# Optimization experiments

Measured on AMD Instinct MI355X. Metric: run time of the kernel, lower is better.

## Reference

```python
import jax, jax.numpy as jnp
import numpy as np

D_MODEL, D_STATE, EXPAND = 256, 16, 2
D_INNER = EXPAND * D_MODEL
DT_RANK = (D_MODEL + 15) // 16
BATCH, SEQLEN = 4, 4096


def silu(x):
    return x * jax.nn.sigmoid(x)


def setup_inputs() -> dict:
    key = jax.random.key(0)
    ks = jax.random.split(key, 10)
    h = jax.random.normal(ks[0], (BATCH, SEQLEN, D_MODEL), dtype=jnp.float32)
    Wi_f = jax.random.normal(ks[1], (2 * D_INNER, D_MODEL), dtype=jnp.float32) / np.sqrt(D_MODEL)
    Wi_b = jax.random.normal(ks[2], (2 * D_INNER, D_MODEL), dtype=jnp.float32) / np.sqrt(D_MODEL)
    Wx_f = jax.random.normal(ks[3], (DT_RANK + 2 * D_STATE, D_INNER), dtype=jnp.float32) / np.sqrt(D_INNER)
    Wx_b = jax.random.normal(ks[4], (DT_RANK + 2 * D_STATE, D_INNER), dtype=jnp.float32) / np.sqrt(D_INNER)
    dt_std = DT_RANK ** -0.5
    Wdt_f = jax.random.uniform(ks[5], (D_INNER, DT_RANK), dtype=jnp.float32, minval=-dt_std, maxval=dt_std)
    Wdt_b = jax.random.uniform(ks[6], (D_INNER, DT_RANK), dtype=jnp.float32, minval=-dt_std, maxval=dt_std)
    # dt bias = inverse-softplus of dt sampled log-uniform in [1e-3, 1e-1]
    dt = jnp.exp(jax.random.uniform(ks[7], (D_INNER,), dtype=jnp.float32) * (np.log(0.1) - np.log(0.001)) + np.log(0.001))
    dt = jnp.clip(dt, 1e-4, None)
    inv_dt = dt + jnp.log(-jnp.expm1(-dt))
    bdt_f = inv_dt
    bdt_b = inv_dt
    A_log = jnp.log(jnp.broadcast_to(jnp.arange(1, D_STATE + 1, dtype=jnp.float32), (D_INNER, D_STATE)))
    A_log_f = A_log
    A_log_b = A_log
    D_f = jnp.ones((D_INNER,), dtype=jnp.float32)
    D_b = jnp.ones((D_INNER,), dtype=jnp.float32)
    Wo = jax.random.normal(ks[8], (D_MODEL, 2 * D_INNER), dtype=jnp.float32) / np.sqrt(2 * D_INNER)
    return {"hidden_states": h, "Wi_f": Wi_f, "Wi_b": Wi_b, "Wx_f": Wx_f, "Wx_b": Wx_b,
            "Wdt_f": Wdt_f, "Wdt_b": Wdt_b, "bdt_f": bdt_f, "bdt_b": bdt_b,
            "A_log_f": A_log_f, "A_log_b": A_log_b, "D_f": D_f, "D_b": D_b, "Wo": Wo}


def mamba_dir(h, Wi, Wx, Wdt, bdt, A_log, Dp, reverse):
    b, l, _ = h.shape
    di, r = Wdt.shape
    n = A_log.shape[1]
    xz = h @ Wi.T                      # [b,l,2*di]
    if reverse:
        xz = xz[:, ::-1]
    x, z = xz[..., :di], xz[..., di:]
    u = silu(x)                        # selective_scan input u
    x_dbl = u @ Wx.T                   # [b,l,r+2n]
    delta = jax.nn.softplus(x_dbl[..., :r] @ Wdt.T + bdt)   # [b,l,di]
    Bm = x_dbl[..., r:r + n]           # [b,l,n]
    Cm = x_dbl[..., r + n:r + 2 * n]   # [b,l,n]
    A = -jnp.exp(A_log)                # [di,n]

    def step(s, inp):
        u_t, d_t, B_t, C_t = inp       # [b,di],[b,di],[b,n],[b,n]
        dA = jnp.exp(d_t[..., None] * A)                         # [b,di,n]
        s = dA * s + (d_t * u_t)[..., None] * B_t[:, None, :]    # [b,di,n]
        y_t = jnp.einsum('bdn,bn->bd', s, C_t)
        return s, y_t

    s0 = jnp.zeros((b, di, n), dtype=u.dtype)
    xs = (jnp.swapaxes(u, 0, 1), jnp.swapaxes(delta, 0, 1),
          jnp.swapaxes(Bm, 0, 1), jnp.swapaxes(Cm, 0, 1))
    _, ys = jax.lax.scan(step, s0, xs)
    y = jnp.swapaxes(ys, 0, 1) + u * Dp          # skip term D*u
    y = y * silu(z)                              # gated output
    if reverse:
        y = y[:, ::-1]
    return y


def reference(hidden_states, Wi_f, Wi_b, Wx_f, Wx_b, Wdt_f, Wdt_b, bdt_f, bdt_b, A_log_f, A_log_b, D_f, D_b, Wo):
    y_f = mamba_dir(hidden_states, Wi_f, Wx_f, Wdt_f, bdt_f, A_log_f, D_f, False)
    y_b = mamba_dir(hidden_states, Wi_b, Wx_b, Wdt_b, bdt_b, A_log_b, D_b, True)
    y = jnp.concatenate([y_f, y_b], axis=-1)     # [b,l,2*di]
    return y @ Wo.T                              # [b,l,d_model]
```

## Files before the change

kernel.cpp:

```cpp
#include <hip/hip_runtime.h>
#include <hip/hip_bf16.h>
#include <cstddef>
#include <cstdint>

#define D_MODELc 256
#define D_STATEc 16
#define D_INNERc 512
#define DT_RANKc 16
#define BATCHc   4
#define SEQLENc  4096
#define NCHUNK   128
#define CHUNK    32

typedef unsigned short u16;
typedef __attribute__((ext_vector_type(8))) short bf16x8;
typedef __attribute__((ext_vector_type(4))) float f32x4;
typedef float __attribute__((ext_vector_type(4))) f4v;

__device__ __forceinline__ float siluf(float v) { return v / (1.f + __expf(-v)); }

__device__ __forceinline__ u16 bf16_rne(float f) {
    uint32_t u = __float_as_uint(f);
    u += 0x7fffu + ((u >> 16) & 1u);
    return (u16)(u >> 16);
}
__device__ __forceinline__ float bf16_to_f(u16 h) {
    return __uint_as_float(((uint32_t)h) << 16);
}
__device__ __forceinline__ uint32_t pack_hl(float f) {
    u16 hh = bf16_rne(f);
    u16 ll = bf16_rne(f - bf16_to_f(hh));
    return ((uint32_t)hh << 16) | ll;
}
__device__ __forceinline__ float unpack_add(uint32_t v) {
    return __uint_as_float(v & 0xFFFF0000u) + __uint_as_float(v << 16);
}
__device__ __forceinline__ void unpack_frag(const uint32_t* q, bf16x8& fh, bf16x8& fl) {
    union { bf16x8 v; uint32_t w[4]; } H, L;
    #pragma unroll
    for (int i = 0; i < 4; i++) {
        uint32_t a = q[2 * i], b = q[2 * i + 1];
        H.w[i] = (a >> 16) | (b & 0xFFFF0000u);
        L.w[i] = (a & 0xFFFFu) | (b << 16);
    }
    fh = H.v; fl = L.v;
}
__device__ __forceinline__ float softplusf(float x) {
    return fmaxf(x, 0.f) + __logf(1.f + __expf(-fabsf(x)));
}
__device__ __forceinline__ float dot16_tree(const f4v x[4], const float* w, float bias) {
    float t0 = fmaf(x[0][1], w[1],  x[0][0] * w[0]);
    float t1 = fmaf(x[0][3], w[3],  x[0][2] * w[2]);
    float t2 = fmaf(x[1][1], w[5],  x[1][0] * w[4]);
    float t3 = fmaf(x[1][3], w[7],  x[1][2] * w[6]);
    float t4 = fmaf(x[2][1], w[9],  x[2][0] * w[8]);
    float t5 = fmaf(x[2][3], w[11], x[2][2] * w[10]);
    float t6 = fmaf(x[3][1], w[13], x[3][2] * 0.f + x[3][0] * w[12]);
    float t7 = fmaf(x[3][3], w[15], x[3][2] * w[14]);
    return bias + (((t0 + t1) + (t2 + t3)) + ((t4 + t5) + (t6 + t7)));
}
__device__ __forceinline__ void qladder(float q, float* qd) {
    float q2 = q * q;
    float q4 = q2 * q2;
    float q8 = q4 * q4;
    qd[0] = q;        qd[1] = q2;       qd[2] = q2 * q;   qd[3] = q4;
    qd[4] = q4 * q;   qd[5] = q4 * q2;  qd[6] = q4 * qd[2]; qd[7] = q8;
    qd[8] = q8 * q;   qd[9] = q8 * q2;  qd[10] = q8 * qd[2]; qd[11] = q8 * q4;
    qd[12] = q8 * qd[4]; qd[13] = q8 * qd[5]; qd[14] = q8 * qd[6]; qd[15] = q8 * q8;
}

#define GLL16(g, l) __builtin_amdgcn_global_load_lds( \
    (const __attribute__((address_space(1))) uint32_t*)(g), \
    (__attribute__((address_space(3))) uint32_t*)(l), 16, 0, 0)

__global__ __launch_bounds__(256) void split_kernel(const float* __restrict__ in,
                                                    u16* __restrict__ hi,
                                                    u16* __restrict__ lo, int n4) {
    int i = blockIdx.x * 256 + threadIdx.x;
    const int stride = gridDim.x * 256;
    for (; i < n4; i += stride) {
        float4 v = ((const float4*)in)[i];
        u16 h0 = bf16_rne(v.x), h1 = bf16_rne(v.y), h2 = bf16_rne(v.z), h3 = bf16_rne(v.w);
        ushort4 hv; hv.x = h0; hv.y = h1; hv.z = h2; hv.w = h3;
        ushort4 lv;
        lv.x = bf16_rne(v.x - bf16_to_f(h0));
        lv.y = bf16_rne(v.y - bf16_to_f(h1));
        lv.z = bf16_rne(v.z - bf16_to_f(h2));
        lv.w = bf16_rne(v.w - bf16_to_f(h3));
        ((ushort4*)hi)[i] = hv;
        ((ushort4*)lo)[i] = lv;
    }
}

template<int EPI, int NBL2, int AINT>
__global__ __launch_bounds__(256) void gemm_mfma(
        const u16* __restrict__ Ah, const u16* __restrict__ Al, int lda,
        const u16* __restrict__ Bh, const u16* __restrict__ Bl, int ldb,
        float* __restrict__ out0,
        uint32_t* __restrict__ uhl,
        int M, int N, int K) {
    __shared__ u16 ldsB[2][2][4][128][8];
    const int t    = threadIdx.x;
    const int lane = t & 63;
    const int wid  = t >> 6;
    const int wrow = wid >> 1, wcol = wid & 1;

    const int id  = blockIdx.x;
    const int xcd = id & 7;
    const int j   = id >> 3;
    const int nb  = j & ((1 << NBL2) - 1);
    const int mg  = j >> NBL2;
    const int m0  = (mg * 8 + xcd) * 128;
    const int n0  = nb * 128;

    const int lr  = lane & 15;
    const int kgl = lane >> 4;

    f32x4 acc[4][4] = {};

    auto stageB = [&](int buf, int k0) {
        #pragma unroll
        for (int i = 0; i < 4; i++) {
            int c    = i * 256 + t;
            int tile = c >> 9;
            int kg   = (c >> 7) & 3;
            int row  = c & 127;
            const u16* bsrc = tile ? Bl : Bh;
            const u16* g = bsrc + (size_t)(n0 + row) * ldb + k0 + kg * 8;
            GLL16(g, ((char*)ldsB) + (size_t)buf * 16384 + (size_t)c * 16);
        }
    };

    const int NT = K >> 5;
    stageB(0, 0);
    __syncthreads();

    for (int kt = 0; kt < NT; ++kt) {
        const int buf = kt & 1;
        if (kt + 1 < NT) stageB(buf ^ 1, (kt + 1) * 32);

        bf16x8 afh[4], afl[4];
        const int k0 = kt * 32;
        #pragma unroll
        for (int mi = 0; mi < 4; mi++) {
            int row = m0 + wrow * 64 + mi * 16 + lr;
            if (AINT == 0) {
                afh[mi] = *(const bf16x8*)(Ah + (size_t)row * lda + k0 + kgl * 8);
                afl[mi] = *(const bf16x8*)(Al + (size_t)row * lda + k0 + kgl * 8);
            } else {
                const uint32_t* Aint = (const uint32_t*)Ah;
                unpack_frag(Aint + (size_t)row * lda + k0 + kgl * 8, afh[mi], afl[mi]);
            }
        }

        #pragma unroll
        for (int ni = 0; ni < 4; ni++) {
            int row = wcol * 64 + ni * 16 + lr;
            bf16x8 bfh = *(const bf16x8*)&ldsB[buf][0][kgl][row][0];
            bf16x8 bfl = *(const bf16x8*)&ldsB[buf][1][kgl][row][0];
            #pragma unroll
            for (int mi = 0; mi < 4; mi++) {
                acc[mi][ni] = __builtin_amdgcn_mfma_f32_16x16x32_bf16(afh[mi], bfh, acc[mi][ni], 0, 0, 0);
                acc[mi][ni] = __builtin_amdgcn_mfma_f32_16x16x32_bf16(afh[mi], bfl, acc[mi][ni], 0, 0, 0);
                acc[mi][ni] = __builtin_amdgcn_mfma_f32_16x16x32_bf16(afl[mi], bfh, acc[mi][ni], 0, 0, 0);
            }
        }
        __syncthreads();
    }

    #pragma unroll
    for (int mi = 0; mi < 4; mi++) {
        #pragma unroll
        for (int ni = 0; ni < 4; ni++) {
            #pragma unroll
            for (int r = 0; r < 4; r++) {
                int m = m0 + wrow * 64 + mi * 16 + kgl * 4 + r;
                int n = n0 + wcol * 64 + ni * 16 + lr;
                float v = acc[mi][ni][r];
                if (EPI == 0) {
                    __builtin_nontemporal_store(v, &out0[(size_t)m * N + n]);
                } else {
                    float s = siluf(v);
                    int dirn = n >> 10;
                    int nn   = n & 1023;
                    size_t dof = (size_t)dirn * (size_t)M * 512;
                    if (nn < 512) {
                        uhl[dof + (size_t)m * 512 + nn] = pack_hl(s);
                    } else {
                        out0[dof + (size_t)m * 512 + (nn - 512)] = s;
                    }
                }
            }
        }
    }
}

__global__ __launch_bounds__(256) void xdbl_mfma(
        const uint32_t* __restrict__ Uhl,
        const u16* __restrict__ WxH, const u16* __restrict__ WxL,
        float* __restrict__ out) {
    __shared__ uint32_t lds[4][64][8];
    const int t    = threadIdx.x;
    const int lane = t & 63;
    const int wid  = t >> 6;
    const int m0   = blockIdx.x * 64;
    const int dir  = blockIdx.y;
    const int Mp   = gridDim.x * 64;
    const int lr   = lane & 15;
    const int kgl  = lane >> 4;

    const size_t dofU = (size_t)dir * (size_t)Mp * 512;
    const size_t dofW = (size_t)dir * (size_t)48 * 512;

    f32x4 acc[3] = {};

    for (int k0 = 0; k0 < 512; k0 += 32) {
        #pragma unroll
        for (int i = 0; i < 2; i++) {
            int c    = i * 256 + t;
            int kg   = c >> 7;
            int row  = (c >> 1) & 63;
            int half = c & 1;
            const uint32_t* g = Uhl + dofU + (size_t)(m0 + row) * 512 + k0 + kg * 8 + half * 4;
            GLL16(g, ((char*)lds) + (size_t)c * 16);
        }
        __syncthreads();

        bf16x8 afh, afl;
        unpack_frag(&lds[kgl][wid * 16 + lr][0], afh, afl);
        #pragma unroll
        for (int nf = 0; nf < 3; nf++) {
            const size_t boff = dofW + (size_t)(nf * 16 + lr) * 512 + k0 + kgl * 8;
            bf16x8 bfh = *(const bf16x8*)(WxH + boff);
            bf16x8 bfl = *(const bf16x8*)(WxL + boff);
            acc[nf] = __builtin_amdgcn_mfma_f32_16x16x32_bf16(afh, bfh, acc[nf], 0, 0, 0);
            acc[nf] = __builtin_amdgcn_mfma_f32_16x16x32_bf16(afh, bfl, acc[nf], 0, 0, 0);
            acc[nf] = __builtin_amdgcn_mfma_f32_16x16x32_bf16(afl, bfh, acc[nf], 0, 0, 0);
        }
        __syncthreads();
    }

    float* o = out + (size_t)dir * (size_t)Mp * 48;
    #pragma unroll
    for (int nf = 0; nf < 3; nf++) {
        #pragma unroll
        for (int r = 0; r < 4; r++) {
            int m = m0 + wid * 16 + kgl * 4 + r;
            int n = nf * 16 + lr;
            o[(size_t)m * 48 + n] = acc[nf][r];
        }
    }
}

__global__ __launch_bounds__(256) void scan_phaseA(
        const uint32_t* __restrict__ Uhl,
        const float* __restrict__ XD,
        const float* __restrict__ Wdt_f, const float* __restrict__ Wdt_b,
        const float* __restrict__ bdt_f, const float* __restrict__ bdt_b,
        const float* __restrict__ AL_f, const float* __restrict__ AL_b,
        float* __restrict__ SDL, float* __restrict__ S) {
    const int c   = blockIdx.x;
    const int d   = blockIdx.y * 256 + threadIdx.x;
    const int z   = blockIdx.z;
    const int dir = z & 1;
    const int b   = z >> 1;
    const int PB  = gridDim.z >> 1;
    const int Mp  = PB * SEQLENc;
    const float* Wdt = dir ? Wdt_b : Wdt_f;
    const float* bdt = dir ? bdt_b : bdt_f;
    const float* AL  = dir ? AL_b  : AL_f;
    const uint32_t* UD = Uhl + (size_t)dir * Mp * 512;
    const float* XDD = XD + (size_t)dir * Mp * 48;

    float w[16], a[16], s[16];
    #pragma unroll
    for (int n = 0; n < 16; n++) {
        w[n] = Wdt[d * 16 + n];
        a[n] = -__expf(AL[d * 16 + n]);
        s[n] = 0.f;
    }
    const float a0 = a[0];
    bool pw = (a0 != 0.f);
    #pragma unroll
    for (int n = 1; n < 16; n++)
        pw = pw && (fabsf(a[n] - (float)(n + 1) * a0) <= 3e-6f * fabsf(a[n]));
    const float bb = bdt[d];
    float sdl = 0.f;

    for (int i = 0; i < CHUNK; i++) {
        int tt = c * CHUNK + i;
        int l  = dir ? (SEQLENc - 1 - tt) : tt;
        size_t row = (size_t)b * SEQLENc + l;
        float uu = unpack_add(UD[row * 512 + d]);
        const f4v* xr4 = (const f4v*)&XDD[row * 48];
        f4v xw[4] = {xr4[0], xr4[1], xr4[2], xr4[3]};
        float dl = softplusf(dot16_tree(xw, w, bb));
        sdl += dl;
        float du = dl * uu;
        if (pw) {
            float qd[16];
            qladder(__expf(a0 * dl), qd);
            #pragma unroll
            for (int g = 0; g < 4; g++) {
                f4v B4 = xr4[4 + g];
                #pragma unroll
                for (int jj = 0; jj < 4; jj++) {
                    int n = g * 4 + jj;
                    s[n] = fmaf(qd[n], s[n], du * B4[jj]);
                }
            }
        } else {
            #pragma unroll
            for (int g = 0; g < 4; g++) {
                f4v B4 = xr4[4 + g];
                #pragma unroll
                for (int jj = 0; jj < 4; jj++) {
                    int n = g * 4 + jj;
                    float dA = __expf(dl * a[n]);
                    s[n] = fmaf(dA, s[n], du * B4[jj]);
                }
            }
        }
    }
    SDL[((size_t)z * NCHUNK + c) * 512 + d] = sdl;
    size_t base = (((size_t)z * NCHUNK + c) * 16) * 512 + d;
    #pragma unroll
    for (int n = 0; n < 16; n++)
        S[base + (size_t)n * 512] = s[n];
}

__global__ __launch_bounds__(256) void scan_phaseB(const float* __restrict__ SDL,
                                                   float* __restrict__ S,
                                                   const float* __restrict__ AL_f,
                                                   const float* __restrict__ AL_b) {
    const int g   = blockIdx.x * 256 + threadIdx.x;
    const int d   = g & 511;
    const int n   = (g >> 9) & 15;
    const int z   = g >> 13;
    const int dir = z & 1;
    const float an = -__expf((dir ? AL_b : AL_f)[d * 16 + n]);
    const size_t strideS = (size_t)16 * 512;
    size_t offS = (((size_t)z * NCHUNK) * 16 + n) * 512 + d;
    size_t offD = ((size_t)z * NCHUNK) * 512 + d;
    float carry = 0.f;
    float sdl = SDL[offD], ss = S[offS];
    for (int c = 0; c < NCHUNK; c++) {
        float sdn = 0.f, sn = 0.f;
        if (c + 1 < NCHUNK) { sdn = SDL[offD + 512]; sn = S[offS + strideS]; }
        float pp = __expf(an * sdl);
        S[offS] = carry;
        carry = pp * carry + ss;
        sdl = sdn; ss = sn;
        offS += strideS; offD += 512;
    }
}

__global__ __launch_bounds__(256) void scan_phaseC(
        const uint32_t* __restrict__ Uhl,
        const float* __restrict__ XD,
        const float* __restrict__ Wdt_f, const float* __restrict__ Wdt_b,
        const float* __restrict__ bdt_f, const float* __restrict__ bdt_b,
        const float* __restrict__ AL_f, const float* __restrict__ AL_b,
        const float* __restrict__ E,
        const float* __restrict__ SZ,
        const float* __restrict__ D_f,  const float* __restrict__ D_b,
        uint32_t* __restrict__ Yhl) {
    const int c   = blockIdx.x;
    const int d   = blockIdx.y * 256 + threadIdx.x;
    const int z   = blockIdx.z;
    const int dir = z & 1;
    const int b   = z >> 1;
    const int PB  = gridDim.z >> 1;
    const int Mp  = PB * SEQLENc;
    const float* Wdt = dir ? Wdt_b : Wdt_f;
    const float* bdt = dir ? bdt_b : bdt_f;
    const float* AL  = dir ? AL_b  : AL_f;
    const uint32_t* UD = Uhl + (size_t)dir * Mp * 512;
    const float* XDD = XD + (size_t)dir * Mp * 48;
    const float* SZD = SZ + (size_t)dir * Mp * 512;

    float w[16], a[16], s[16];
    size_t base = (((size_t)z * NCHUNK + c) * 16) * 512 + d;
    #pragma unroll
    for (int n = 0; n < 16; n++) {
        w[n] = Wdt[d * 16 + n];
        a[n] = -__expf(AL[d * 16 + n]);
        s[n] = E[base + (size_t)n * 512];
    }
    const float a0 = a[0];
    bool pw = (a0 != 0.f);
    #pragma unroll
    for (int n = 1; n < 16; n++)
        pw = pw && (fabsf(a[n] - (float)(n + 1) * a0) <= 3e-6f * fabsf(a[n]));
    const float bb = bdt[d];
    const float Dd = (dir ? D_b : D_f)[d];

    for (int i = 0; i < CHUNK; i++) {
        int tt = c * CHUNK + i;
        int l  = dir ? (SEQLENc - 1 - tt) : tt;
        size_t row = (size_t)b * SEQLENc + l;
        float uu = unpack_add(UD[row * 512 + d]);
        const f4v* xr4 = (const f4v*)&XDD[row * 48];
        f4v xw[4] = {xr4[0], xr4[1], xr4[2], xr4[3]};
        float dl = softplusf(dot16_tree(xw, w, bb));
        float du = dl * uu;
        float yp0 = 0.f, yp1 = 0.f, yp2 = 0.f, yp3 = 0.f;
        if (pw) {
            float qd[16];
            qladder(__expf(a0 * dl), qd);
            #pragma unroll
            for (int g = 0; g < 4; g++) {
                f4v B4 = xr4[4 + g];
                f4v C4 = xr4[8 + g];
                float yp = 0.f;
                #pragma unroll
                for (int jj = 0; jj < 4; jj++) {
                    int n = g * 4 + jj;
                    s[n] = fmaf(qd[n], s[n], du * B4[jj]);
                    yp = fmaf(s[n], C4[jj], yp);
                }
                if (g == 0) yp0 = yp; else if (g == 1) yp1 = yp;
                else if (g == 2) yp2 = yp; else yp3 = yp;
            }
        } else {
            #pragma unroll
            for (int g = 0; g < 4; g++) {
                f4v B4 = xr4[4 + g];
                f4v C4 = xr4[8 + g];
                float yp = 0.f;
                #pragma unroll
                for (int jj = 0; jj < 4; jj++) {
                    int n = g * 4 + jj;
                    float dA = __expf(dl * a[n]);
                    s[n] = fmaf(dA, s[n], du * B4[jj]);
                    yp = fmaf(s[n], C4[jj], yp);
                }
                if (g == 0) yp0 = yp; else if (g == 1) yp1 = yp;
                else if (g == 2) yp2 = yp; else yp3 = yp;
            }
        }
        float y = (yp0 + yp1) + (yp2 + yp3);
        float sz = SZD[row * 512 + d];
        float yv = (y + uu * Dd) * sz;
        Yhl[row * 1024 + (size_t)dir * 512 + d] = pack_hl(yv);
    }
}

extern "C" void kernel_launch(void* const* d_in, const int* in_sizes, int n_in,
                              void* d_out, int out_size, void* d_ws, size_t ws_size,
                              hipStream_t stream) {
    const float* h    = (const float*)d_in[0];
    const float* Wi_f = (const float*)d_in[1];
    const float* Wi_b = (const float*)d_in[2];
    const float* Wx_f = (const float*)d_in[3];
    const float* Wx_b = (const float*)d_in[4];
    const float* Wdt_f= (const float*)d_in[5];
    const float* Wdt_b= (const float*)d_in[6];
    const float* bdt_f= (const float*)d_in[7];
    const float* bdt_b= (const float*)d_in[8];
    const float* Al_f = (const float*)d_in[9];
    const float* Al_b = (const float*)d_in[10];
    const float* D_f  = (const float*)d_in[11];
    const float* D_b  = (const float*)d_in[12];
    const float* Wo   = (const float*)d_in[13];
    float* out = (float*)d_out;

    const size_t W_ELE  = 1024 * 256;
    const size_t WX_ELE = 48 * 512;
    const size_t FB   = (size_t)SEQLENc * D_INNERc;
    const size_t FH   = (size_t)SEQLENc * D_MODELc;
    const size_t FX   = (size_t)SEQLENc * 48;
    const size_t FP   = (size_t)NCHUNK * 16 * 512;
    const size_t FD   = (size_t)NCHUNK * 512;
    const size_t FY   = (size_t)SEQLENc * 1024;

    const size_t fixed_bytes = (8 * W_ELE + 4 * WX_ELE) * sizeof(u16);
    const size_t per_b = 2 * FH * sizeof(u16)
                       + 2 * FB * sizeof(float)
                       + 2 * FB * sizeof(uint32_t)
                       + 2 * FX * sizeof(float)
                       + 2 * (FP + FD) * sizeof(float)
                       + FY * sizeof(uint32_t);
    int PB = 4;
    if (fixed_bytes + 4 * per_b + 65536 > ws_size) PB = 2;
    if (fixed_bytes + 2 * per_b + 65536 > ws_size) PB = 1;

    char* cur = (char*)d_ws;
    auto alloc = [&](size_t bytes) -> char* {
        char* p = cur; cur += (bytes + 255) & ~(size_t)255; return p;
    };
    u16* WiH = (u16*)alloc(2 * W_ELE * 2);
    u16* WiL = (u16*)alloc(2 * W_ELE * 2);
    u16* WoH = (u16*)alloc(W_ELE * 2);
    u16* WoL = (u16*)alloc(W_ELE * 2);
    u16* WxH = (u16*)alloc(2 * WX_ELE * 2);
    u16* WxL = (u16*)alloc(2 * WX_ELE * 2);
    u16*      hH  = (u16*)alloc((size_t)PB * FH * 2);
    u16*      hL  = (u16*)alloc((size_t)PB * FH * 2);
    float*    sz  = (float*)alloc((size_t)PB * 2 * FB * 4);
    uint32_t* uhl = (uint32_t*)alloc((size_t)PB * 2 * FB * 4);
    float*    xd  = (float*)alloc((size_t)PB * 2 * FX * 4);
    float*    SDL = (float*)alloc((size_t)PB * 2 * FD * 4);
    float*    S   = (float*)alloc((size_t)PB * 2 * FP * 4);
    uint32_t* yhl = (uint32_t*)alloc((size_t)PB * FY * 4);

    {
        int n4 = (int)(W_ELE / 4);
        int blocks = (n4 + 255) / 256; if (blocks > 1024) blocks = 1024;
        split_kernel<<<blocks, 256, 0, stream>>>(Wi_f, WiH, WiL, n4);
        split_kernel<<<blocks, 256, 0, stream>>>(Wi_b, WiH + W_ELE, WiL + W_ELE, n4);
        split_kernel<<<blocks, 256, 0, stream>>>(Wo,   WoH, WoL, n4);
        int nx4 = (int)(WX_ELE / 4);
        split_kernel<<<(nx4 + 255) / 256, 256, 0, stream>>>(Wx_f, WxH, WxL, nx4);
        split_kernel<<<(nx4 + 255) / 256, 256, 0, stream>>>(Wx_b, WxH + WX_ELE, WxL + WX_ELE, nx4);
    }

    for (int b0 = 0; b0 < BATCHc; b0 += PB) {
        const int Mp = PB * SEQLENc;
        const int MB = Mp / 128;
        const float* hB = h   + (size_t)b0 * FH;
        float*       oB = out + (size_t)b0 * FH;

        {
            int n4 = (int)((size_t)PB * FH / 4);
            int blocks = (n4 + 255) / 256; if (blocks > 2048) blocks = 2048;
            split_kernel<<<blocks, 256, 0, stream>>>(hB, hH, hL, n4);
        }

        gemm_mfma<1, 4, 0><<<16 * MB, 256, 0, stream>>>(
            hH, hL, D_MODELc, WiH, WiL, D_MODELc,
            sz, uhl, Mp, 2048, D_MODELc);

        xdbl_mfma<<<dim3(Mp / 64, 2), 256, 0, stream>>>(uhl, WxH, WxL, xd);

        scan_phaseA<<<dim3(NCHUNK, 2, 2 * PB), 256, 0, stream>>>(
            uhl, xd, Wdt_f, Wdt_b, bdt_f, bdt_b, Al_f, Al_b, SDL, S);
        scan_phaseB<<<PB * 64, 256, 0, stream>>>(SDL, S, Al_f, Al_b);
        scan_phaseC<<<dim3(NCHUNK, 2, 2 * PB), 256, 0, stream>>>(
            uhl, xd, Wdt_f, Wdt_b, bdt_f, bdt_b, Al_f, Al_b,
            S, sz, D_f, D_b, yhl);

        gemm_mfma<0, 1, 1><<<2 * MB, 256, 0, stream>>>(
            (const u16*)yhl, nullptr, 1024, WoH, WoL, 1024,
            oB, nullptr, Mp, D_MODELc, 1024);
    }
}
```

Before: 389.7 us.

## Stage A operand through LDS via async loads and merge weight split launches

```diff
diff --git a/kernel.cpp b/kernel.cpp
--- a/kernel.cpp
+++ b/kernel.cpp
@@ -55,7 +55,7 @@
     float t3 = fmaf(x[1][3], w[7],  x[1][2] * w[6]);
     float t4 = fmaf(x[2][1], w[9],  x[2][0] * w[8]);
     float t5 = fmaf(x[2][3], w[11], x[2][2] * w[10]);
-    float t6 = fmaf(x[3][1], w[13], x[3][2] * 0.f + x[3][0] * w[12]);
+    float t6 = fmaf(x[3][1], w[13], x[3][0] * w[12]);
     float t7 = fmaf(x[3][3], w[15], x[3][2] * w[14]);
     return bias + (((t0 + t1) + (t2 + t3)) + ((t4 + t5) + (t6 + t7)));
 }
@@ -63,7 +63,7 @@
     float q2 = q * q;
     float q4 = q2 * q2;
     float q8 = q4 * q4;
-    qd[0] = q;        qd[1] = q2;       qd[2] = q2 * q;   qd[3] = q4;
+    qd[0] = q;        qd[1] = q2;       qd[2] = q2 * q;     qd[3] = q4;
     qd[4] = q4 * q;   qd[5] = q4 * q2;  qd[6] = q4 * qd[2]; qd[7] = q8;
     qd[8] = q8 * q;   qd[9] = q8 * q2;  qd[10] = q8 * qd[2]; qd[11] = q8 * q4;
     qd[12] = q8 * qd[4]; qd[13] = q8 * qd[5]; qd[14] = q8 * qd[6]; qd[15] = q8 * q8;
@@ -72,6 +72,37 @@
 #define GLL16(g, l) __builtin_amdgcn_global_load_lds( \
     (const __attribute__((address_space(1))) uint32_t*)(g), \
     (__attribute__((address_space(3))) uint32_t*)(l), 16, 0, 0)
+
+__global__ __launch_bounds__(256) void split5_kernel(
+        const float* __restrict__ s0, const float* __restrict__ s1,
+        const float* __restrict__ s2, const float* __restrict__ s3,
+        const float* __restrict__ s4,
+        u16* __restrict__ h0, u16* __restrict__ l0,
+        u16* __restrict__ h1, u16* __restrict__ l1,
+        u16* __restrict__ h2, u16* __restrict__ l2,
+        u16* __restrict__ h3, u16* __restrict__ l3,
+        u16* __restrict__ h4, u16* __restrict__ l4,
+        int n4w, int n4x) {
+    const int which = blockIdx.y;
+    const float* in; u16* hi; u16* lo; int n4;
+    if      (which == 0) { in = s0; hi = h0; lo = l0; n4 = n4w; }
+    else if (which == 1) { in = s1; hi = h1; lo = l1; n4 = n4w; }
+    else if (which == 2) { in = s2; hi = h2; lo = l2; n4 = n4w; }
+    else if (which == 3) { in = s3; hi = h3; lo = l3; n4 = n4x; }
+    else                 { in = s4; hi = h4; lo = l4; n4 = n4x; }
+    for (int i = blockIdx.x * 256 + threadIdx.x; i < n4; i += gridDim.x * 256) {
+        float4 v = ((const float4*)in)[i];
+        u16 a0 = bf16_rne(v.x), a1 = bf16_rne(v.y), a2 = bf16_rne(v.z), a3 = bf16_rne(v.w);
+        ushort4 hv; hv.x = a0; hv.y = a1; hv.z = a2; hv.w = a3;
+        ushort4 lv;
+        lv.x = bf16_rne(v.x - bf16_to_f(a0));
+        lv.y = bf16_rne(v.y - bf16_to_f(a1));
+        lv.z = bf16_rne(v.z - bf16_to_f(a2));
+        lv.w = bf16_rne(v.w - bf16_to_f(a3));
+        ((ushort4*)hi)[i] = hv;
+        ((ushort4*)lo)[i] = lv;
+    }
+}
 
 __global__ __launch_bounds__(256) void split_kernel(const float* __restrict__ in,
                                                     u16* __restrict__ hi,
@@ -80,13 +111,13 @@
     const int stride = gridDim.x * 256;
     for (; i < n4; i += stride) {
         float4 v = ((const float4*)in)[i];
-        u16 h0 = bf16_rne(v.x), h1 = bf16_rne(v.y), h2 = bf16_rne(v.z), h3 = bf16_rne(v.w);
-        ushort4 hv; hv.x = h0; hv.y = h1; hv.z = h2; hv.w = h3;
+        u16 a0 = bf16_rne(v.x), a1 = bf16_rne(v.y), a2 = bf16_rne(v.z), a3 = bf16_rne(v.w);
+        ushort4 hv; hv.x = a0; hv.y = a1; hv.z = a2; hv.w = a3;
         ushort4 lv;
-        lv.x = bf16_rne(v.x - bf16_to_f(h0));
-        lv.y = bf16_rne(v.y - bf16_to_f(h1));
-        lv.z = bf16_rne(v.z - bf16_to_f(h2));
-        lv.w = bf16_rne(v.w - bf16_to_f(h3));
+        lv.x = bf16_rne(v.x - bf16_to_f(a0));
+        lv.y = bf16_rne(v.y - bf16_to_f(a1));
+        lv.z = bf16_rne(v.z - bf16_to_f(a2));
+        lv.w = bf16_rne(v.w - bf16_to_f(a3));
         ((ushort4*)hi)[i] = hv;
         ((ushort4*)lo)[i] = lv;
     }
@@ -99,7 +130,7 @@
         float* __restrict__ out0,
         uint32_t* __restrict__ uhl,
         int M, int N, int K) {
-    __shared__ u16 ldsB[2][2][4][128][8];
+    __shared__ char lds[2][32768];
     const int t    = threadIdx.x;
     const int lane = t & 63;
     const int wid  = t >> 6;
@@ -118,46 +149,75 @@
 
     f32x4 acc[4][4] = {};
 
-    auto stageB = [&](int buf, int k0) {
-        #pragma unroll
-        for (int i = 0; i < 4; i++) {
-            int c    = i * 256 + t;
-            int tile = c >> 9;
-            int kg   = (c >> 7) & 3;
-            int row  = c & 127;
-            const u16* bsrc = tile ? Bl : Bh;
-            const u16* g = bsrc + (size_t)(n0 + row) * ldb + k0 + kg * 8;
-            GLL16(g, ((char*)ldsB) + (size_t)buf * 16384 + (size_t)c * 16);
+    auto stage = [&](int buf, int k0) {
+        if (AINT == 0) {
+            #pragma unroll
+            for (int i = 0; i < 8; i++) {
+                int c    = i * 256 + t;
+                int tile = c >> 9;
+                int kg   = (c >> 7) & 3;
+                int row  = c & 127;
+                const u16* bsrc = (tile == 0) ? Ah : (tile == 1) ? Al : (tile == 2) ? Bh : Bl;
+                int r0 = (tile < 2) ? m0 : n0;
+                int ld = (tile < 2) ? lda : ldb;
+                const u16* g = bsrc + (size_t)(r0 + row) * ld + k0 + kg * 8;
+                GLL16(g, &lds[buf][c * 16]);
+            }
+        } else {
+            const uint32_t* Aint = (const uint32_t*)Ah;
+            #pragma unroll
+            for (int i = 0; i < 8; i++) {
+                int c = i * 256 + t;
+                if (c < 1024) {
+                    int kg   = c >> 8;
+                    int row  = (c >> 1) & 127;
+                    int half = c & 1;
+                    const uint32_t* g = Aint + (size_t)(m0 + row) * lda + k0 + kg * 8 + half * 4;
+                    GLL16(g, &lds[buf][c * 16]);
+                } else {
+                    int cb   = c - 1024;
+                    int tile = cb >> 9;
+                    int kg   = (cb >> 7) & 3;
+                    int row  = cb & 127;
+                    const u16* bsrc = tile ? Bl : Bh;
+                    const u16* g = bsrc + (size_t)(n0 + row) * ldb + k0 + kg * 8;
+                    GLL16(g, &lds[buf][c * 16]);
+                }
+            }
         }
     };
 
     const int NT = K >> 5;
-    stageB(0, 0);
+    stage(0, 0);
     __syncthreads();
 
     for (int kt = 0; kt < NT; ++kt) {
         const int buf = kt & 1;
-        if (kt + 1 < NT) stageB(buf ^ 1, (kt + 1) * 32);
+        if (kt + 1 < NT) stage(buf ^ 1, (kt + 1) * 32);
 
         bf16x8 afh[4], afl[4];
-        const int k0 = kt * 32;
-        #pragma unroll
-        for (int mi = 0; mi < 4; mi++) {
-            int row = m0 + wrow * 64 + mi * 16 + lr;
-            if (AINT == 0) {
-                afh[mi] = *(const bf16x8*)(Ah + (size_t)row * lda + k0 + kgl * 8);
-                afl[mi] = *(const bf16x8*)(Al + (size_t)row * lda + k0 + kgl * 8);
-            } else {
-                const uint32_t* Aint = (const uint32_t*)Ah;
-                unpack_frag(Aint + (size_t)row * lda + k0 + kgl * 8, afh[mi], afl[mi]);
-            }
-        }
-
+        if (AINT == 0) {
+            const u16* lb = (const u16*)lds[buf];
+            #pragma unroll
+            for (int mi = 0; mi < 4; mi++) {
+                int row = wrow * 64 + mi * 16 + lr;
+                afh[mi] = *(const bf16x8*)(lb + 0 * 4096 + kgl * 1024 + row * 8);
+                afl[mi] = *(const bf16x8*)(lb + 1 * 4096 + kgl * 1024 + row * 8);
+            }
+        } else {
+            const uint32_t* la = (const uint32_t*)lds[buf];
+            #pragma unroll
+            for (int mi = 0; mi < 4; mi++) {
+                int row = wrow * 64 + mi * 16 + lr;
+                unpack_frag(la + kgl * 1024 + row * 8, afh[mi], afl[mi]);
+            }
+        }
+        const u16* lbB = (const u16*)(lds[buf] + 16384);
         #pragma unroll
         for (int ni = 0; ni < 4; ni++) {
             int row = wcol * 64 + ni * 16 + lr;
-            bf16x8 bfh = *(const bf16x8*)&ldsB[buf][0][kgl][row][0];
-            bf16x8 bfl = *(const bf16x8*)&ldsB[buf][1][kgl][row][0];
+            bf16x8 bfh = *(const bf16x8*)(lbB + 0 * 4096 + kgl * 1024 + row * 8);
+            bf16x8 bfl = *(const bf16x8*)(lbB + 1 * 4096 + kgl * 1024 + row * 8);
             #pragma unroll
             for (int mi = 0; mi < 4; mi++) {
                 acc[mi][ni] = __builtin_amdgcn_mfma_f32_16x16x32_bf16(afh[mi], bfh, acc[mi][ni], 0, 0, 0);
@@ -505,14 +565,13 @@
     uint32_t* yhl = (uint32_t*)alloc((size_t)PB * FY * 4);
 
     {
-        int n4 = (int)(W_ELE / 4);
-        int blocks = (n4 + 255) / 256; if (blocks > 1024) blocks = 1024;
-        split_kernel<<<blocks, 256, 0, stream>>>(Wi_f, WiH, WiL, n4);
-        split_kernel<<<blocks, 256, 0, stream>>>(Wi_b, WiH + W_ELE, WiL + W_ELE, n4);
-        split_kernel<<<blocks, 256, 0, stream>>>(Wo,   WoH, WoL, n4);
-        int nx4 = (int)(WX_ELE / 4);
-        split_kernel<<<(nx4 + 255) / 256, 256, 0, stream>>>(Wx_f, WxH, WxL, nx4);
-        split_kernel<<<(nx4 + 255) / 256, 256, 0, stream>>>(Wx_b, WxH + WX_ELE, WxL + WX_ELE, nx4);
+        int n4w = (int)(W_ELE / 4);
+        int n4x = (int)(WX_ELE / 4);
+        split5_kernel<<<dim3(64, 5), 256, 0, stream>>>(
+            Wi_f, Wi_b, Wo, Wx_f, Wx_b,
+            WiH, WiL, WiH + W_ELE, WiL + W_ELE, WoH, WoL,
+            WxH, WxL, WxH + WX_ELE, WxL + WX_ELE,
+            n4w, n4x);
     }
 
     for (int b0 = 0; b0 < BATCHc; b0 += PB) {
```

Measured after the change: 345.7 us. 1.13x faster.
